# Kernel tuning notes

Hardware: AMD Instinct MI355X
Metric: run time of the kernel (lower is better)

The kernel has to match this reference:

```python
import jax, jax.numpy as jnp
import numpy as np

BETA = 0.25  # commitment loss weight (beta)
EPS_NORM = 1e-12  # F.normalize eps


def l2norm(t):
    return t / jnp.clip(jnp.linalg.norm(t, axis=-1, keepdims=True), EPS_NORM)


def setup_inputs() -> dict:
    key = jax.random.key(0)
    k1, k2 = jax.random.split(key)
    z = jax.random.normal(k1, (16, 256, 32, 32), dtype=jnp.float32)
    # EmbeddingEMA with kmeans_init=False: weight = l2norm(randn(n_embed, dim))
    weight = l2norm(jax.random.normal(k2, (8192, 256), dtype=jnp.float32))
    return {"z": z, "weight": weight}


def reference(z, weight):
    # z: [B, C, H, W] -> [B, H, W, C], l2-normalized per token
    zc = l2norm(jnp.transpose(z, (0, 2, 3, 1)))
    B, H, W, D = zc.shape
    zf = zc.reshape(-1, D)  # [N, D]
    zf_d = jax.lax.stop_gradient(zf)
    # negative squared L2 distance: -|z|^2 - |w|^2 + 2 z.w  -> argmax = nearest code
    d = (-jnp.sum(zf_d ** 2, axis=1, keepdims=True)
         - jnp.sum(weight ** 2, axis=1)
         + 2.0 * jnp.einsum('nd,kd->nk', zf_d, weight))  # [N, K]
    idx = jnp.argmax(d, axis=1)  # [N]
    z_q = weight[idx].reshape(B, H, W, D)  # codebook gather
    # commitment loss: beta * mean((sg(z_q) - z)^2)
    loss = BETA * jnp.mean((jax.lax.stop_gradient(z_q) - zc) ** 2)
    # straight-through estimator
    z_q = zc + jax.lax.stop_gradient(z_q - zc)
    z_q = jnp.transpose(z_q, (0, 3, 1, 2))  # back to [B, C, H, W]
    return z_q, loss, idx
```

## Files before the change

kernel.cpp:

```cpp
#include <hip/hip_runtime.h>
#include <math.h>

#define BB   16
#define CC   256
#define HW   1024
#define NN   16384
#define DD   256
#define KK   8192
#define ZQ_SIZE 4194304
#define MARGIN 0.017f
#define GCAP 8192
#define RSPLIT 8

typedef __attribute__((ext_vector_type(8))) short short8;
typedef __attribute__((ext_vector_type(4))) float f32x4;

static __device__ inline unsigned short f2bf(float x) {
    unsigned int u = __float_as_uint(x);
    unsigned int r = (u + 0x7fff + ((u >> 16) & 1)) >> 16;
    return (unsigned short)r;
}

static __device__ inline unsigned long long pack_key(float s, int k) {
    unsigned int bits = __float_as_uint(s);
    unsigned int o = (bits & 0x80000000u) ? ~bits : (bits | 0x80000000u);
    return ((unsigned long long)o << 32) | (unsigned int)(~k);
}

__global__ __launch_bounds__(256) void wsqwb_kernel(const float* __restrict__ W,
                                                    float* __restrict__ wsq,
                                                    unsigned short* __restrict__ wb,
                                                    int* __restrict__ gcnt,
                                                    int* __restrict__ oflow) {
    if (blockIdx.x == 0) {
        gcnt[threadIdx.x] = 0;
        if (threadIdx.x == 0) *oflow = 0;
    }
    {
        const int lane = threadIdx.x & 63;
        const int k = blockIdx.x * 4 + (threadIdx.x >> 6);
        float4 v = *(const float4*)(W + (size_t)k * DD + lane * 4);
        float s = v.x * v.x + v.y * v.y + v.z * v.z + v.w * v.w;
        #pragma unroll
        for (int off = 32; off; off >>= 1) s += __shfl_down(s, off);
        if (lane == 0) wsq[k] = s;
    }
    if (blockIdx.x < 1024) {
        const int ch = blockIdx.x * 256 + threadIdx.x;
        const int c = (ch >> 7) & 7;
        const int r = ch & 127;
        const int kt = ch >> 12, dc = (ch >> 10) & 3;
        const int k = kt * 128 + r;
        const int d0 = dc * 64 + c * 8;
        const float4 v0 = *(const float4*)(W + (size_t)k * DD + d0);
        const float4 v1 = *(const float4*)(W + (size_t)k * DD + d0 + 4);
        uint4 out;
        out.x = (unsigned int)f2bf(v0.x) | ((unsigned int)f2bf(v0.y) << 16);
        out.y = (unsigned int)f2bf(v0.z) | ((unsigned int)f2bf(v0.w) << 16);
        out.z = (unsigned int)f2bf(v1.x) | ((unsigned int)f2bf(v1.y) << 16);
        out.w = (unsigned int)f2bf(v1.z) | ((unsigned int)f2bf(v1.w) << 16);
        *(uint4*)(wb + (size_t)ch * 8) = out;
    }
}

__global__ __launch_bounds__(256) void normalize_kernel(const float* __restrict__ z,
                                                        float* __restrict__ zn,
                                                        float* __restrict__ znsq,
                                                        unsigned short* __restrict__ zb) {
    __shared__ float tile[64][257];
    __shared__ float s_nrm[64];
    const int t   = threadIdx.x;
    const int b   = blockIdx.x >> 4;
    const int hw0 = (blockIdx.x & 15) * 64;

    #pragma unroll
    for (int cg = 0; cg < 16; ++cg) {
        int c  = cg * 16 + (t >> 4);
        int hw = (t & 15) * 4;
        float4 v = *(const float4*)(z + ((size_t)(b * CC + c) << 10) + hw0 + hw);
        tile[hw + 0][c] = v.x;
        tile[hw + 1][c] = v.y;
        tile[hw + 2][c] = v.z;
        tile[hw + 3][c] = v.w;
    }
    __syncthreads();
    if (t < 64) {
        float s = 0.f;
        #pragma unroll 8
        for (int c = 0; c < 256; ++c) { float v = tile[t][c]; s += v * v; }
        float nrm = sqrtf(s);
        nrm = fmaxf(nrm, 1e-12f);
        s_nrm[t] = nrm;
        znsq[(size_t)b * HW + hw0 + t] = s / (nrm * nrm);
    }
    __syncthreads();
    const int n0 = b * HW + hw0;
    for (int r = 0; r < 64; ++r) {
        zn[(size_t)(n0 + r) * DD + t] = tile[r][t] / s_nrm[r];
    }
    const int r    = t & 63;
    const int mt   = n0 >> 7;
    const int rg   = (n0 & 127) + r;
    const float nrm = s_nrm[r];
    #pragma unroll
    for (int loop = 0; loop < 8; ++loop) {
        int comb = loop * 4 + (t >> 6);
        int dc = comb >> 3, c = comb & 7;
        int d0 = dc * 64 + c * 8;
        uint4 out;
        out.x = (unsigned int)f2bf(tile[r][d0 + 0] / nrm) | ((unsigned int)f2bf(tile[r][d0 + 1] / nrm) << 16);
        out.y = (unsigned int)f2bf(tile[r][d0 + 2] / nrm) | ((unsigned int)f2bf(tile[r][d0 + 3] / nrm) << 16);
        out.z = (unsigned int)f2bf(tile[r][d0 + 4] / nrm) | ((unsigned int)f2bf(tile[r][d0 + 5] / nrm) << 16);
        out.w = (unsigned int)f2bf(tile[r][d0 + 6] / nrm) | ((unsigned int)f2bf(tile[r][d0 + 7] / nrm) << 16);
        *(uint4*)(zb + (size_t)(mt * 4 + dc) * 8192 + (size_t)(c * 128 + rg) * 8) = out;
    }
}

__global__ __launch_bounds__(256) void score_kernel(const unsigned short* __restrict__ zb,
                                                    const unsigned short* __restrict__ wb,
                                                    const float* __restrict__ wsqv,
                                                    float* __restrict__ cmax) {
    __shared__ unsigned short sA[8192];
    __shared__ unsigned short sB[8192];
    __shared__ float rowbuf[128][4];
    __shared__ __align__(16) float swsq[128];

    const int tid  = threadIdx.x;
    const int w    = tid >> 6;
    const int lane = tid & 63;
    const int wcr  = w >> 1;
    const int wct  = w & 1;
    const int q    = lane >> 4, c15 = lane & 15;
    const int kt   = blockIdx.x & 63;
    const int mt   = blockIdx.x >> 6;

    if (tid < 128) swsq[tid] = wsqv[kt * 128 + tid];

    f32x4 acc[4][4];
    #pragma unroll
    for (int fi = 0; fi < 4; ++fi)
        #pragma unroll
        for (int fj = 0; fj < 4; ++fj)
            acc[fi][fj] = (f32x4){0.f, 0.f, 0.f, 0.f};

    for (int dc = 0; dc < 4; ++dc) {
        const unsigned short* gA = zb + (size_t)(mt * 4 + dc) * 8192;
        const unsigned short* gB = wb + (size_t)(kt * 4 + dc) * 8192;
        #pragma unroll
        for (int i = 0; i < 4; ++i) {
            int eo = ((w * 4 + i) << 9);
            __builtin_amdgcn_global_load_lds(
                (const __attribute__((address_space(1))) void*)(gA + eo + lane * 8),
                (__attribute__((address_space(3))) void*)(sA + eo), 16, 0, 0);
            __builtin_amdgcn_global_load_lds(
                (const __attribute__((address_space(1))) void*)(gB + eo + lane * 8),
                (__attribute__((address_space(3))) void*)(sB + eo), 16, 0, 0);
        }
        __syncthreads();
        #pragma unroll
        for (int ks = 0; ks < 2; ++ks) {
            short8 tfr[4], cfr[4];
            const int ca = (ks * 4 + q) * 128;
            #pragma unroll
            for (int f = 0; f < 4; ++f) {
                tfr[f] = *(const short8*)(sA + (size_t)(ca + wct * 64 + f * 16 + c15) * 8);
                cfr[f] = *(const short8*)(sB + (size_t)(ca + wcr * 64 + f * 16 + c15) * 8);
            }
            #pragma unroll
            for (int fi = 0; fi < 4; ++fi)
                #pragma unroll
                for (int fj = 0; fj < 4; ++fj)
                    acc[fi][fj] = __builtin_amdgcn_mfma_f32_16x16x32_bf16(
                        cfr[fi], tfr[fj], acc[fi][fj], 0, 0, 0);
        }
        __syncthreads();
    }

    f32x4 wq4[4];
    #pragma unroll
    for (int fi = 0; fi < 4; ++fi)
        wq4[fi] = *(const f32x4*)(&swsq[wcr * 64 + fi * 16 + q * 4]);

    #pragma unroll
    for (int fj = 0; fj < 4; ++fj) {
        float g[2];
        #pragma unroll
        for (int p = 0; p < 2; ++p) {
            float vm = -INFINITY;
            #pragma unroll
            for (int f2 = 0; f2 < 2; ++f2) {
                int fi = p * 2 + f2;
                #pragma unroll
                for (int rg = 0; rg < 4; ++rg)
                    vm = fmaxf(vm, 2.0f * acc[fi][fj][rg] - wq4[fi][rg]);
            }
            vm = fmaxf(vm, __shfl_xor(vm, 16));
            vm = fmaxf(vm, __shfl_xor(vm, 32));
            g[p] = vm;
        }
        if (q == 0) {
            int row = wct * 64 + fj * 16 + c15;
            rowbuf[row][wcr * 2 + 0] = g[0];
            rowbuf[row][wcr * 2 + 1] = g[1];
        }
    }
    __syncthreads();
    {
        int row = tid >> 1, half = tid & 1;
        float2 v2 = make_float2(rowbuf[row][half * 2], rowbuf[row][half * 2 + 1]);
        *(float2*)(cmax + (size_t)(mt * 128 + row) * 256 + kt * 4 + half * 2) = v2;
    }
}

__global__ __launch_bounds__(256) void cand_kernel(const float* __restrict__ cmax,
                                                   unsigned int* __restrict__ gseg,
                                                   int* __restrict__ gcnt,
                                                   unsigned long long* __restrict__ packed,
                                                   int* __restrict__ nflag,
                                                   int* __restrict__ oflow) {
    const int t = threadIdx.x, wv = t >> 6, lane = t & 63;
    const int n = blockIdx.x * 4 + wv;
    float4 c4 = *(const float4*)(cmax + (size_t)n * 256 + lane * 4);
    float lm = fmaxf(fmaxf(c4.x, c4.y), fmaxf(c4.z, c4.w));
    #pragma unroll
    for (int off = 1; off <= 32; off <<= 1) lm = fmaxf(lm, __shfl_xor(lm, off));
    const float thresh = lm - MARGIN;
    if (lane == 0) { packed[n] = 0ull; nflag[n] = 0; }
    float g4[4] = {c4.x, c4.y, c4.z, c4.w};
    #pragma unroll
    for (int j = 0; j < 4; ++j) {
        int g = lane * 4 + j;
        if (g4[j] >= thresh) {
            int pos = atomicAdd(&gcnt[g], 1);
            if (pos < GCAP) gseg[(size_t)g * GCAP + pos] = (unsigned int)n;
            else { nflag[n] = 1; atomicAdd(oflow, 1); }
        }
    }
}

__global__ __launch_bounds__(256) void rescore_kernel(const float* __restrict__ zn,
                                                      const float* __restrict__ W,
                                                      const float* __restrict__ wsqv,
                                                      const float* __restrict__ znsq,
                                                      const unsigned int* __restrict__ gseg,
                                                      const int* __restrict__ gcnt,
                                                      unsigned long long* __restrict__ packed) {
    __shared__ float sW[32 * 260];
    __shared__ float znr[4][2][256];

    const int t = threadIdx.x;
    const int g   = blockIdx.x >> 3;
    const int sub = blockIdx.x & 7;
    int cnt = gcnt[g]; if (cnt > GCAP) cnt = GCAP;
    if (cnt <= sub * 8) return;

    {
        int c = t >> 3, i = t & 7;
        const float4* src = (const float4*)(W + (size_t)g * 8192 + c * 256 + i * 32);
        #pragma unroll
        for (int j = 0; j < 8; ++j)
            *(float4*)(sW + c * 260 + i * 32 + j * 4) = src[j];
    }
    __syncthreads();

    const int wv = t >> 6, lane = t & 63;
    const int h = lane >> 5, c = lane & 31;
    const int k = g * 32 + c;
    const float wq = wsqv[k];
    const float4* wrow = (const float4*)(sW + c * 260);

    for (int base = (sub * 4 + wv) * 2; base < cnt; base += RSPLIT * 8) {
        int idx = base + h; if (idx >= cnt) idx = base;
        int n = (int)gseg[(size_t)g * GCAP + idx];
        *(float4*)(&znr[wv][h][c * 8])     = *(const float4*)(zn + (size_t)n * DD + c * 8);
        *(float4*)(&znr[wv][h][c * 8 + 4]) = *(const float4*)(zn + (size_t)n * DD + c * 8 + 4);
        float d = 0.f;
        #pragma unroll
        for (int j = 0; j < 64; ++j) {
            float4 wv4 = wrow[j];
            float4 zv  = *(const float4*)(&znr[wv][h][j * 4]);
            d += wv4.x * zv.x + wv4.y * zv.y + wv4.z * zv.z + wv4.w * zv.w;
        }
        float s = (-znsq[n] - wq) + 2.0f * d;
        unsigned long long key = pack_key(s, k);
        #pragma unroll
        for (int off = 1; off <= 16; off <<= 1) {
            unsigned long long ok = __shfl_xor(key, off);
            if (ok > key) key = ok;
        }
        if (c == 0) atomicMax(packed + n, key);
    }
}

__global__ __launch_bounds__(256) void fullscan_kernel(const float* __restrict__ zn,
                                                       const float* __restrict__ W,
                                                       const float* __restrict__ wsqv,
                                                       const float* __restrict__ znsq,
                                                       const int* __restrict__ nflag,
                                                       const int* __restrict__ oflow,
                                                       unsigned long long* __restrict__ packed) {
    if (*oflow == 0) return;
    const int t = threadIdx.x, wv = t >> 6, lane = t & 63;
    const int code = lane >> 1, part = lane & 1;
    for (int n = blockIdx.x * 4 + wv; n < NN; n += gridDim.x * 4) {
        if (!nflag[n]) continue;
        float zsq = znsq[n];
        unsigned long long best = 0ull;
        for (int gg = 0; gg < 256; ++gg) {
            int k = gg * 32 + code;
            const float4* wrp = (const float4*)(W + (size_t)k * DD + part * 128);
            const float4* zrp = (const float4*)(zn + (size_t)n * DD + part * 128);
            float d = 0.f;
            #pragma unroll
            for (int jj = 0; jj < 32; ++jj) {
                float4 a = zrp[jj], b = wrp[jj];
                d += a.x * b.x + a.y * b.y + a.z * b.z + a.w * b.w;
            }
            d += __shfl_xor(d, 1);
            unsigned long long key = pack_key((-zsq - wsqv[k]) + 2.0f * d, k);
            if (key > best) best = key;
        }
        #pragma unroll
        for (int off = 1; off <= 32; off <<= 1) {
            unsigned long long ok = __shfl_xor(best, off);
            if (ok > best) best = ok;
        }
        if (lane == 0) atomicMax(packed + n, best);
    }
}

__global__ __launch_bounds__(256) void gatherfin_kernel(const float* __restrict__ W,
                                                        const unsigned long long* __restrict__ packed,
                                                        float* __restrict__ idxf,
                                                        float* __restrict__ partials,
                                                        float* __restrict__ zq) {
    __shared__ int sbk[64];
    const int t   = threadIdx.x;
    const int b   = blockIdx.x >> 4;
    const int hw0 = (blockIdx.x & 15) * 64;
    if (t < 64) {
        int n = b * HW + hw0 + t;
        unsigned long long key = packed[n];
        int k = (int)((~(unsigned int)key) & 0x3FFFu);
        unsigned int o = (unsigned int)(key >> 32);
        unsigned int bits = (o & 0x80000000u) ? (o & 0x7FFFFFFFu) : ~o;
        float s = __uint_as_float(bits);
        sbk[t] = k;
        idxf[n] = (float)k;
        float cc = -s;
        #pragma unroll
        for (int off = 32; off; off >>= 1) cc += __shfl_down(cc, off);
        if (t == 0) partials[blockIdx.x] = cc;
    }
    __syncthreads();
    const int hw  = t & 63;
    const int c0  = (t >> 6) * 4;
    const int row = sbk[hw];
    #pragma unroll
    for (int cg = 0; cg < 16; ++cg) {
        int c = cg * 16 + c0;
        float4 v = *(const float4*)(W + (size_t)row * DD + c);
        size_t base = ((size_t)(b * CC + c) << 10) + hw0 + hw;
        zq[base]        = v.x;
        zq[base + 1024] = v.y;
        zq[base + 2048] = v.z;
        zq[base + 3072] = v.w;
    }
}

__global__ __launch_bounds__(256) void loss_final_kernel(const float* __restrict__ partials,
                                                         float* __restrict__ out_loss) {
    __shared__ float wsum[4];
    const int t = threadIdx.x;
    float v = partials[t];
    #pragma unroll
    for (int off = 32; off; off >>= 1) v += __shfl_down(v, off);
    if ((t & 63) == 0) wsum[t >> 6] = v;
    __syncthreads();
    if (t == 0) {
        float tot = wsum[0] + wsum[1] + wsum[2] + wsum[3];
        *out_loss = 0.25f * (tot / (float)ZQ_SIZE);
    }
}

extern "C" void kernel_launch(void* const* d_in, const int* in_sizes, int n_in,
                              void* d_out, int out_size, void* d_ws, size_t ws_size,
                              hipStream_t stream) {
    const float* z = (const float*)d_in[0];
    const float* W = (const float*)d_in[1];

    float* out   = (float*)d_out;
    float* zq    = out;
    float* loss  = out + ZQ_SIZE;
    float* idxf  = out + ZQ_SIZE + 1;

    float* ws       = (float*)d_ws;
    float* zn       = ws;
    float* znsq     = zn + (size_t)NN * DD;
    float* wsqv     = znsq + NN;
    float* partials = wsqv + KK;
    int*   gcnt     = (int*)(partials + 256);
    int*   oflow    = gcnt + 256;
    int*   nflag    = oflow + 64;
    unsigned short* zb = (unsigned short*)(nflag + NN);
    unsigned short* wb = zb + (size_t)NN * DD;
    float* cmax     = (float*)(wb + (size_t)KK * DD);
    unsigned int* gseg = (unsigned int*)(cmax + (size_t)NN * 256);
    unsigned long long* packed = (unsigned long long*)(gseg + (size_t)256 * GCAP);

    wsqwb_kernel     <<<KK / 4, 256, 0, stream>>>(W, wsqv, wb, gcnt, oflow);
    normalize_kernel <<<BB * 16, 256, 0, stream>>>(z, zn, znsq, zb);
    score_kernel     <<<(NN / 128) * (KK / 128), 256, 0, stream>>>(zb, wb, wsqv, cmax);
    cand_kernel      <<<NN / 4, 256, 0, stream>>>(cmax, gseg, gcnt, packed, nflag, oflow);
    rescore_kernel   <<<256 * RSPLIT, 256, 0, stream>>>(zn, W, wsqv, znsq, gseg, gcnt, packed);
    fullscan_kernel  <<<64, 256, 0, stream>>>(zn, W, wsqv, znsq, nflag, oflow, packed);
    gatherfin_kernel <<<BB * 16, 256, 0, stream>>>(W, packed, idxf, partials, zq);
    loss_final_kernel<<<1, 256, 0, stream>>>(partials, loss);
}
```

Measured before the change: 234.3 us.

## Merge prep kernels and fold fullscan and loss reduction into gather kernel

Merges the codebook norm/bf16 conversion kernel and the z normalization kernel into one launch with block-range dispatch. Moves the overflow fallback full scan into the gather kernel, where it works per tile in shared memory, and replaces the final loss-reduction kernel with atomicAdd into the loss output, zeroed in cand_kernel. This cuts the launch count from eight to five to reduce launch and tail overhead. The trade-offs are a nondeterministic float atomic summation order and a heavier gather kernel whenever overflow happens.

```diff
diff --git a/kernel.cpp b/kernel.cpp
--- a/kernel.cpp
+++ b/kernel.cpp
@@ -27,51 +27,55 @@
     return ((unsigned long long)o << 32) | (unsigned int)(~k);
 }
 
-__global__ __launch_bounds__(256) void wsqwb_kernel(const float* __restrict__ W,
-                                                    float* __restrict__ wsq,
-                                                    unsigned short* __restrict__ wb,
-                                                    int* __restrict__ gcnt,
-                                                    int* __restrict__ oflow) {
-    if (blockIdx.x == 0) {
-        gcnt[threadIdx.x] = 0;
-        if (threadIdx.x == 0) *oflow = 0;
-    }
-    {
-        const int lane = threadIdx.x & 63;
-        const int k = blockIdx.x * 4 + (threadIdx.x >> 6);
-        float4 v = *(const float4*)(W + (size_t)k * DD + lane * 4);
-        float s = v.x * v.x + v.y * v.y + v.z * v.z + v.w * v.w;
-        #pragma unroll
-        for (int off = 32; off; off >>= 1) s += __shfl_down(s, off);
-        if (lane == 0) wsq[k] = s;
-    }
-    if (blockIdx.x < 1024) {
-        const int ch = blockIdx.x * 256 + threadIdx.x;
-        const int c = (ch >> 7) & 7;
-        const int r = ch & 127;
-        const int kt = ch >> 12, dc = (ch >> 10) & 3;
-        const int k = kt * 128 + r;
-        const int d0 = dc * 64 + c * 8;
-        const float4 v0 = *(const float4*)(W + (size_t)k * DD + d0);
-        const float4 v1 = *(const float4*)(W + (size_t)k * DD + d0 + 4);
-        uint4 out;
-        out.x = (unsigned int)f2bf(v0.x) | ((unsigned int)f2bf(v0.y) << 16);
-        out.y = (unsigned int)f2bf(v0.z) | ((unsigned int)f2bf(v0.w) << 16);
-        out.z = (unsigned int)f2bf(v1.x) | ((unsigned int)f2bf(v1.y) << 16);
-        out.w = (unsigned int)f2bf(v1.z) | ((unsigned int)f2bf(v1.w) << 16);
-        *(uint4*)(wb + (size_t)ch * 8) = out;
-    }
-}
-
-__global__ __launch_bounds__(256) void normalize_kernel(const float* __restrict__ z,
-                                                        float* __restrict__ zn,
-                                                        float* __restrict__ znsq,
-                                                        unsigned short* __restrict__ zb) {
+__global__ __launch_bounds__(256) void prep_kernel(const float* __restrict__ W,
+                                                   const float* __restrict__ z,
+                                                   float* __restrict__ wsq,
+                                                   unsigned short* __restrict__ wb,
+                                                   float* __restrict__ zn,
+                                                   float* __restrict__ znsq,
+                                                   unsigned short* __restrict__ zb,
+                                                   int* __restrict__ gcnt,
+                                                   int* __restrict__ oflow) {
     __shared__ float tile[64][257];
     __shared__ float s_nrm[64];
-    const int t   = threadIdx.x;
-    const int b   = blockIdx.x >> 4;
-    const int hw0 = (blockIdx.x & 15) * 64;
+    const int t = threadIdx.x;
+
+    if (blockIdx.x < 2048) {
+        if (blockIdx.x == 0) {
+            gcnt[t] = 0;
+            if (t == 0) *oflow = 0;
+        }
+        {
+            const int lane = t & 63;
+            const int k = blockIdx.x * 4 + (t >> 6);
+            float4 v = *(const float4*)(W + (size_t)k * DD + lane * 4);
+            float s = v.x * v.x + v.y * v.y + v.z * v.z + v.w * v.w;
+            #pragma unroll
+            for (int off = 32; off; off >>= 1) s += __shfl_down(s, off);
+            if (lane == 0) wsq[k] = s;
+        }
+        if (blockIdx.x < 1024) {
+            const int ch = blockIdx.x * 256 + t;
+            const int c = (ch >> 7) & 7;
+            const int r = ch & 127;
+            const int kt = ch >> 12, dc = (ch >> 10) & 3;
+            const int k = kt * 128 + r;
+            const int d0 = dc * 64 + c * 8;
+            const float4 v0 = *(const float4*)(W + (size_t)k * DD + d0);
+            const float4 v1 = *(const float4*)(W + (size_t)k * DD + d0 + 4);
+            uint4 o;
+            o.x = (unsigned int)f2bf(v0.x) | ((unsigned int)f2bf(v0.y) << 16);
+            o.y = (unsigned int)f2bf(v0.z) | ((unsigned int)f2bf(v0.w) << 16);
+            o.z = (unsigned int)f2bf(v1.x) | ((unsigned int)f2bf(v1.y) << 16);
+            o.w = (unsigned int)f2bf(v1.z) | ((unsigned int)f2bf(v1.w) << 16);
+            *(uint4*)(wb + (size_t)ch * 8) = o;
+        }
+        return;
+    }
+
+    const int bx  = blockIdx.x - 2048;
+    const int b   = bx >> 4;
+    const int hw0 = (bx & 15) * 64;
 
     #pragma unroll
     for (int cg = 0; cg < 16; ++cg) {
@@ -217,9 +221,11 @@
                                                    int* __restrict__ gcnt,
                                                    unsigned long long* __restrict__ packed,
                                                    int* __restrict__ nflag,
-                                                   int* __restrict__ oflow) {
+                                                   int* __restrict__ oflow,
+                                                   float* __restrict__ loss_out) {
     const int t = threadIdx.x, wv = t >> 6, lane = t & 63;
     const int n = blockIdx.x * 4 + wv;
+    if (blockIdx.x == 0 && t == 0) *loss_out = 0.f;
     float4 c4 = *(const float4*)(cmax + (size_t)n * 256 + lane * 4);
     float lm = fmaxf(fmaxf(c4.x, c4.y), fmaxf(c4.z, c4.w));
     #pragma unroll
@@ -292,67 +298,75 @@
     }
 }
 
-__global__ __launch_bounds__(256) void fullscan_kernel(const float* __restrict__ zn,
-                                                       const float* __restrict__ W,
-                                                       const float* __restrict__ wsqv,
-                                                       const float* __restrict__ znsq,
-                                                       const int* __restrict__ nflag,
-                                                       const int* __restrict__ oflow,
-                                                       unsigned long long* __restrict__ packed) {
-    if (*oflow == 0) return;
-    const int t = threadIdx.x, wv = t >> 6, lane = t & 63;
-    const int code = lane >> 1, part = lane & 1;
-    for (int n = blockIdx.x * 4 + wv; n < NN; n += gridDim.x * 4) {
-        if (!nflag[n]) continue;
-        float zsq = znsq[n];
-        unsigned long long best = 0ull;
-        for (int gg = 0; gg < 256; ++gg) {
-            int k = gg * 32 + code;
-            const float4* wrp = (const float4*)(W + (size_t)k * DD + part * 128);
-            const float4* zrp = (const float4*)(zn + (size_t)n * DD + part * 128);
-            float d = 0.f;
-            #pragma unroll
-            for (int jj = 0; jj < 32; ++jj) {
-                float4 a = zrp[jj], b = wrp[jj];
-                d += a.x * b.x + a.y * b.y + a.z * b.z + a.w * b.w;
-            }
-            d += __shfl_xor(d, 1);
-            unsigned long long key = pack_key((-zsq - wsqv[k]) + 2.0f * d, k);
-            if (key > best) best = key;
-        }
-        #pragma unroll
-        for (int off = 1; off <= 32; off <<= 1) {
-            unsigned long long ok = __shfl_xor(best, off);
-            if (ok > best) best = ok;
-        }
-        if (lane == 0) atomicMax(packed + n, best);
-    }
-}
-
 __global__ __launch_bounds__(256) void gatherfin_kernel(const float* __restrict__ W,
+                                                        const float* __restrict__ zn,
+                                                        const float* __restrict__ wsqv,
+                                                        const float* __restrict__ znsq,
                                                         const unsigned long long* __restrict__ packed,
+                                                        const int* __restrict__ nflag,
+                                                        const int* __restrict__ oflow,
                                                         float* __restrict__ idxf,
-                                                        float* __restrict__ partials,
+                                                        float* __restrict__ loss_out,
                                                         float* __restrict__ zq) {
+    __shared__ unsigned long long skey[64];
     __shared__ int sbk[64];
+    __shared__ int flg[64];
     const int t   = threadIdx.x;
+    const int wv  = t >> 6, lane = t & 63;
     const int b   = blockIdx.x >> 4;
     const int hw0 = (blockIdx.x & 15) * 64;
+    const int n0  = b * HW + hw0;
+
+    if (t < 64) skey[t] = packed[n0 + t];
+
+    if (*oflow != 0) {
+        if (t < 64) flg[t] = nflag[n0 + t];
+        __syncthreads();
+        const int code = lane >> 1, part = lane & 1;
+        for (int i = wv; i < 64; i += 4) {
+            if (!flg[i]) continue;
+            int n = n0 + i;
+            float zsq = znsq[n];
+            unsigned long long best = 0ull;
+            for (int gg = 0; gg < 256; ++gg) {
+                int k = gg * 32 + code;
+                const float4* wrp = (const float4*)(W + (size_t)k * DD + part * 128);
+                const float4* zrp = (const float4*)(zn + (size_t)n * DD + part * 128);
+                float d = 0.f;
+                #pragma unroll
+                for (int jj = 0; jj < 32; ++jj) {
+                    float4 a = zrp[jj], bb = wrp[jj];
+                    d += a.x * bb.x + a.y * bb.y + a.z * bb.z + a.w * bb.w;
+                }
+                d += __shfl_xor(d, 1);
+                unsigned long long key = pack_key((-zsq - wsqv[k]) + 2.0f * d, k);
+                if (key > best) best = key;
+            }
+            #pragma unroll
+            for (int off = 1; off <= 32; off <<= 1) {
+                unsigned long long ok = __shfl_xor(best, off);
+                if (ok > best) best = ok;
+            }
+            if (lane == 0 && best > skey[i]) skey[i] = best;
+        }
+    }
+    __syncthreads();
+
     if (t < 64) {
-        int n = b * HW + hw0 + t;
-        unsigned long long key = packed[n];
+        unsigned long long key = skey[t];
         int k = (int)((~(unsigned int)key) & 0x3FFFu);
         unsigned int o = (unsigned int)(key >> 32);
         unsigned int bits = (o & 0x80000000u) ? (o & 0x7FFFFFFFu) : ~o;
         float s = __uint_as_float(bits);
         sbk[t] = k;
-        idxf[n] = (float)k;
+        idxf[n0 + t] = (float)k;
         float cc = -s;
         #pragma unroll
         for (int off = 32; off; off >>= 1) cc += __shfl_down(cc, off);
-        if (t == 0) partials[blockIdx.x] = cc;
-    }
-    __syncthreads();
+        if (t == 0) atomicAdd(loss_out, 0.25f * (cc / (float)ZQ_SIZE));
+    }
+    __syncthreads();
+
     const int hw  = t & 63;
     const int c0  = (t >> 6) * 4;
     const int row = sbk[hw];
@@ -368,21 +382,6 @@
     }
 }
 
-__global__ __launch_bounds__(256) void loss_final_kernel(const float* __restrict__ partials,
-                                                         float* __restrict__ out_loss) {
-    __shared__ float wsum[4];
-    const int t = threadIdx.x;
-    float v = partials[t];
-    #pragma unroll
-    for (int off = 32; off; off >>= 1) v += __shfl_down(v, off);
-    if ((t & 63) == 0) wsum[t >> 6] = v;
-    __syncthreads();
-    if (t == 0) {
-        float tot = wsum[0] + wsum[1] + wsum[2] + wsum[3];
-        *out_loss = 0.25f * (tot / (float)ZQ_SIZE);
-    }
-}
-
 extern "C" void kernel_launch(void* const* d_in, const int* in_sizes, int n_in,
                               void* d_out, int out_size, void* d_ws, size_t ws_size,
                               hipStream_t stream) {
@@ -398,8 +397,7 @@
     float* zn       = ws;
     float* znsq     = zn + (size_t)NN * DD;
     float* wsqv     = znsq + NN;
-    float* partials = wsqv + KK;
-    int*   gcnt     = (int*)(partials + 256);
+    int*   gcnt     = (int*)(wsqv + KK);
     int*   oflow    = gcnt + 256;
     int*   nflag    = oflow + 64;
     unsigned short* zb = (unsigned short*)(nflag + NN);
@@ -408,12 +406,10 @@
     unsigned int* gseg = (unsigned int*)(cmax + (size_t)NN * 256);
     unsigned long long* packed = (unsigned long long*)(gseg + (size_t)256 * GCAP);
 
-    wsqwb_kernel     <<<KK / 4, 256, 0, stream>>>(W, wsqv, wb, gcnt, oflow);
-    normalize_kernel <<<BB * 16, 256, 0, stream>>>(z, zn, znsq, zb);
+    prep_kernel      <<<2048 + 256, 256, 0, stream>>>(W, z, wsqv, wb, zn, znsq, zb, gcnt, oflow);
     score_kernel     <<<(NN / 128) * (KK / 128), 256, 0, stream>>>(zb, wb, wsqv, cmax);
-    cand_kernel      <<<NN / 4, 256, 0, stream>>>(cmax, gseg, gcnt, packed, nflag, oflow);
+    cand_kernel      <<<NN / 4, 256, 0, stream>>>(cmax, gseg, gcnt, packed, nflag, oflow, loss);
     rescore_kernel   <<<256 * RSPLIT, 256, 0, stream>>>(zn, W, wsqv, znsq, gseg, gcnt, packed);
-    fullscan_kernel  <<<64, 256, 0, stream>>>(zn, W, wsqv, znsq, nflag, oflow, packed);
-    gatherfin_kernel <<<BB * 16, 256, 0, stream>>>(W, packed, idxf, partials, zq);
-    loss_final_kernel<<<1, 256, 0, stream>>>(partials, loss);
-}
+    gatherfin_kernel <<<BB * 16, 256, 0, stream>>>(W, zn, wsqv, znsq, packed, nflag, oflow,
+                                                   idxf, loss, zq);
+}
```

Result: slower. 242.0 us (+3.3%).
